# Performance work log

Hardware: AMD Instinct MI355X
Metric: run time of the kernel (lower is better)

Reference implementation:

```python
import jax, jax.numpy as jnp
import numpy as np

DIM = 128; MOTION = 128; HEADS = 8; WS = 8; B2 = 4; H = 192; W = 192; HID = 512

def _ln(x, w, b, eps=1e-5):
    m = x.mean(-1, keepdims=True)
    v = ((x - m) ** 2).mean(-1, keepdims=True)
    return (x - m) / jnp.sqrt(v + eps) * w + b

def _win_part(x, ws):
    B, Hh, Ww, C = x.shape
    x = x.reshape(B, Hh // ws, ws, Ww // ws, ws, C).transpose(0, 1, 3, 2, 4, 5)
    return x.reshape(-1, ws * ws, C)

def _win_rev(win, ws, Hh, Ww):
    nwB, N, C = win.shape
    B = nwB // ((Hh // ws) * (Ww // ws))
    x = win.reshape(B, Hh // ws, Ww // ws, ws, ws, C).transpose(0, 1, 3, 2, 4, 5)
    return x.reshape(B, Hh, Ww, C)

def setup_inputs() -> dict:
    key = jax.random.key(0)
    ks = jax.random.split(key, 12)
    def lin(k, o, i):
        return jax.random.normal(k, (o, i), jnp.float32) * 0.02
    return {
        "x": jax.random.normal(ks[0], (B2, H * W, DIM), jnp.float32),
        "cor": jax.random.uniform(ks[1], (B2, H * W, 2), dtype=jnp.float32),
        "q_w": lin(ks[2], DIM, DIM),
        "kv_w": lin(ks[3], 2 * DIM, DIM),
        "cor_w": lin(ks[4], MOTION, 2),
        "proj_w": lin(ks[5], DIM, DIM), "proj_b": jnp.zeros((DIM,), jnp.float32),
        "mproj_w": lin(ks[6], MOTION, MOTION), "mproj_b": jnp.zeros((MOTION,), jnp.float32),
        "norm1_w": jnp.ones((DIM,), jnp.float32), "norm1_b": jnp.zeros((DIM,), jnp.float32),
        "norm2_w": jnp.ones((DIM,), jnp.float32), "norm2_b": jnp.zeros((DIM,), jnp.float32),
        "fc1_w": lin(ks[7], HID, DIM), "fc1_b": jnp.zeros((HID,), jnp.float32),
        "dw_w": jax.random.normal(ks[8], (HID, 1, 3, 3), jnp.float32) * 0.1,
        "dw_b": jnp.zeros((HID,), jnp.float32),
        "fc2_w": lin(ks[9], DIM, HID), "fc2_b": jnp.zeros((DIM,), jnp.float32),
    }

def _attn(x1, x2, cor, q_w, kv_w, cor_w, proj_w, proj_b, mproj_w, mproj_b):
    # x1,x2: (nwB, N, C) windowed query / cross-frame key-value; cor: (nwB, N, 2)
    B, N, C = x1.shape
    hd = C // HEADS
    mh = MOTION // HEADS
    scale = hd ** -0.5
    q = (x1 @ q_w.T).reshape(B, N, HEADS, hd).transpose(0, 2, 1, 3)
    kv = (x2 @ kv_w.T).reshape(B, N, 2, HEADS, hd).transpose(2, 0, 3, 1, 4)
    k, v = kv[0], kv[1]
    ce = cor @ cor_w.T                                   # (B, N, MOTION)
    ceh = ce.reshape(B, N, HEADS, mh).transpose(0, 2, 1, 3)
    attn = jax.nn.softmax(jnp.einsum('bhnd,bhmd->bhnm', q, k) * scale, axis=-1)
    xo = jnp.einsum('bhnm,bhmd->bhnd', attn, v).transpose(0, 2, 1, 3).reshape(B, N, C)
    crev = jnp.einsum('bhnm,bhmd->bhnd', attn, ceh).transpose(0, 2, 1, 3).reshape(B, N, MOTION)
    motion = (crev - ce) @ mproj_w.T + mproj_b
    return xo @ proj_w.T + proj_b, motion

def _mlp(x, fc1_w, fc1_b, dw_w, dw_b, fc2_w, fc2_b):
    B, N, _ = x.shape
    h = x @ fc1_w.T + fc1_b                              # (B, N, HID)
    hm = h.transpose(0, 2, 1).reshape(B, HID, H, W)
    hm = jax.lax.conv_general_dilated(hm, dw_w, (1, 1), 'SAME',
                                      feature_group_count=HID,
                                      dimension_numbers=('NCHW', 'OIHW', 'NCHW'))
    hm = hm + dw_b[None, :, None, None]
    h = jax.nn.gelu(hm.reshape(B, HID, N).transpose(0, 2, 1), approximate=False)
    return h @ fc2_w.T + fc2_b

def reference(x, cor, q_w, kv_w, cor_w, proj_w, proj_b, mproj_w, mproj_b,
              norm1_w, norm1_b, norm2_w, norm2_b, fc1_w, fc1_b, dw_w, dw_b, fc2_w, fc2_b):
    shortcut = x
    xn = _ln(x, norm1_w, norm1_b).reshape(B2, H, W, DIM)
    cm = cor.reshape(B2, H, W, 2)
    xw = _win_part(xn, WS)                               # (nwB, 64, DIM)
    cw = _win_part(cm, WS)
    nwB = xw.shape[0]
    xr = jnp.concatenate([xw[nwB // 2:], xw[:nwB // 2]], axis=0)
    xa, xm = _attn(xw, xr, cw, q_w, kv_w, cor_w, proj_w, proj_b, mproj_w, mproj_b)
    xa = _win_rev(xa, WS, H, W).reshape(B2, H * W, DIM)
    xm = _win_rev(xm, WS, H, W).reshape(B2, H * W, MOTION)
    x = shortcut + xa
    x = x + _mlp(_ln(x, norm2_w, norm2_b), fc1_w, fc1_b, dw_w, dw_b, fc2_w, fc2_b)
    return x, xm
```

## Files before the change

### kernel.cpp

```cpp
#include <hip/hip_runtime.h>
#include <hip/hip_bf16.h>
#include <math.h>

#define NB 4
#define IMG 192
#define HW (IMG*IMG)
#define T_TOT (NB*HW)
#define HID 512
#define NWB 2304
#define WPB 576
#define NWS 24

typedef __bf16 bf16;
typedef __bf16 bf8 __attribute__((ext_vector_type(8)));
typedef __bf16 bf4 __attribute__((ext_vector_type(4)));
typedef float f32x4 __attribute__((ext_vector_type(4)));

#define MFMA(a,b,c) __builtin_amdgcn_mfma_f32_16x16x32_bf16(a,b,c,0,0,0)

__device__ __forceinline__ int swz128(int row, int col){ return row*128 + (col ^ ((row&7)<<3)); }

__device__ __forceinline__ bf8 zero_bf8(){
  bf8 z = { (bf16)0.f,(bf16)0.f,(bf16)0.f,(bf16)0.f,(bf16)0.f,(bf16)0.f,(bf16)0.f,(bf16)0.f };
  return z;
}
__device__ __forceinline__ f32x4 zero_f4(){ f32x4 z = {0.f,0.f,0.f,0.f}; return z; }

__global__ void k_cvt(const float* __restrict__ s, bf16* __restrict__ d, int n, float scale){
  int i = blockIdx.x*256 + threadIdx.x;
  if (i < n) d[i] = (bf16)(s[i]*scale);
}

__global__ void k_a2(const float* __restrict__ mproj_w, const float* __restrict__ cor_w,
                     bf16* __restrict__ a2w){
  int idx = blockIdx.x*256 + threadIdx.x;
  if (idx >= 4096) return;
  int o = idx >> 5, k = idx & 31;
  float acc = 0.f;
  if (k < 16){
    int h = k >> 1, c = k & 1;
    #pragma unroll
    for (int i=0;i<16;i++)
      acc += mproj_w[o*128 + h*16 + i] * cor_w[(h*16+i)*2 + c];
  }
  a2w[o*32 + k] = (bf16)acc;
}

__global__ __launch_bounds__(256) void k_ln1(
    const float* __restrict__ x, const float* __restrict__ cor,
    const float* __restrict__ n1w, const float* __restrict__ n1b,
    bf16* __restrict__ xn, bf16* __restrict__ cwb)
{
  int tid = threadIdx.x, wm = tid>>6, l = tid&63;
  int lr = l & 15, tg = l >> 4;
  int t = blockIdx.x*16 + wm*4 + tg;

  const float* xp = x + (size_t)t*128 + lr*8;
  float4 a = *(const float4*)xp;
  float4 b4 = *(const float4*)(xp+4);
  float s  = a.x+a.y+a.z+a.w + b4.x+b4.y+b4.z+b4.w;
  float sq = a.x*a.x+a.y*a.y+a.z*a.z+a.w*a.w + b4.x*b4.x+b4.y*b4.y+b4.z*b4.z+b4.w*b4.w;
  #pragma unroll
  for (int m=1;m<16;m<<=1){ s += __shfl_xor(s,m,16); sq += __shfl_xor(sq,m,16); }
  float mean = s * (1.0f/128.0f);
  float var  = sq * (1.0f/128.0f) - mean*mean;
  float rstd = rsqrtf(var + 1e-5f);

  float4 nw0 = *(const float4*)(n1w + lr*8), nw1 = *(const float4*)(n1w + lr*8 + 4);
  float4 nb0 = *(const float4*)(n1b + lr*8), nb1 = *(const float4*)(n1b + lr*8 + 4);

  bf8 o;
  o[0] = (bf16)((a.x -mean)*rstd*nw0.x + nb0.x);
  o[1] = (bf16)((a.y -mean)*rstd*nw0.y + nb0.y);
  o[2] = (bf16)((a.z -mean)*rstd*nw0.z + nb0.z);
  o[3] = (bf16)((a.w -mean)*rstd*nw0.w + nb0.w);
  o[4] = (bf16)((b4.x-mean)*rstd*nw1.x + nb1.x);
  o[5] = (bf16)((b4.y-mean)*rstd*nw1.y + nb1.y);
  o[6] = (bf16)((b4.z-mean)*rstd*nw1.z + nb1.z);
  o[7] = (bf16)((b4.w-mean)*rstd*nw1.w + nb1.w);

  int b = t / HW, r = t % HW;
  int yy = r / IMG, xx = r % IMG;
  int win = b*WPB + (yy>>3)*NWS + (xx>>3);
  int n = ((yy&7)<<3) + (xx&7);
  *(bf8*)(xn + (size_t)win*8192 + n*128 + lr*8) = o;

  if (lr < 2) cwb[(size_t)win*128 + n*2 + lr] = (bf16)cor[(size_t)t*2 + lr];
}

__global__ __launch_bounds__(256) void k_attn(
    const bf16* __restrict__ xn, const bf16* __restrict__ cw,
    const bf16* __restrict__ wq, const bf16* __restrict__ wkv,
    const bf16* __restrict__ wpj, const bf16* __restrict__ a2w,
    const float* __restrict__ proj_b, const float* __restrict__ mproj_b,
    const float* __restrict__ x_in, float* __restrict__ x1, float* __restrict__ out_m)
{
  __shared__ __align__(16) bf16 s_s [64*128];
  __shared__ __align__(16) bf16 s_k [64*128];
  __shared__ __align__(16) bf16 s_vT[128*64];
  __shared__ __align__(16) bf16 s_P [2][64*64];
  __shared__ __align__(16) bf16 s_cT[16*64];
  __shared__ __align__(16) bf16 s_D [64*32];

  int tid = threadIdx.x, wm = tid>>6, l = tid&63;
  int lr = l & 15, lg = l >> 4;
  int win = blockIdx.x;
  int partner = (win + NWB/2) % NWB;
  const bf16* xw_g = xn + (size_t)win*8192;
  const bf16* xr_g = xn + (size_t)partner*8192;

  bf8 xrv[4], xwv[4];
  #pragma unroll
  for (int tci=0;tci<4;tci++){
    int chunk = tid + tci*256;
    int row = chunk>>4, c0 = (chunk&15)*8;
    xrv[tci] = *(const bf8*)(xr_g + row*128 + c0);
    xwv[tci] = *(const bf8*)(xw_g + row*128 + c0);
  }
  bf16 cwv = (bf16)0.f;
  if (tid < 128) cwv = cw[(size_t)win*128 + tid];

  *(unsigned long long*)&s_cT[tid*4] = 0ull;
  *(unsigned long long*)&s_D[tid*8]   = 0ull;
  *(unsigned long long*)&s_D[tid*8+4] = 0ull;
  #pragma unroll
  for (int tci=0;tci<4;tci++){
    int chunk = tid + tci*256;
    int row = chunk>>4, c0 = (chunk&15)*8;
    *(bf8*)&s_s[swz128(row,c0)] = xrv[tci];
  }
  __syncthreads();

  if (tid < 128){
    int c = tid & 1, m = tid >> 1;
    s_cT[c*64 + (m ^ (c<<3))] = cwv;
  } else if (tid < 192){
    int m = tid - 128;
    s_cT[2*64 + (m ^ 16)] = (bf16)1.0f;
  }
  {
    bf8 af[4];
    #pragma unroll
    for (int ks=0;ks<4;ks++) af[ks] = *(const bf8*)&s_s[swz128(wm*16+lr, ks*32 + lg*8)];
    #pragma unroll
    for (int nt=0;nt<8;nt++){
      f32x4 acc = zero_f4();
      #pragma unroll
      for (int ks=0;ks<4;ks++){
        bf8 bfr = *(const bf8*)(wkv + (nt*16+lr)*128 + ks*32 + lg*8);
        acc = MFMA(af[ks], bfr, acc);
      }
      #pragma unroll
      for (int j=0;j<4;j++){
        int row = wm*16 + lg*4 + j;
        s_k[swz128(row, nt*16+lr)] = (bf16)acc[j];
      }
    }
    #pragma unroll
    for (int nt=0;nt<8;nt++){
      f32x4 acc = zero_f4();
      #pragma unroll
      for (int ks=0;ks<4;ks++){
        bf8 bfr = *(const bf8*)(wkv + (128 + nt*16+lr)*128 + ks*32 + lg*8);
        acc = MFMA(af[ks], bfr, acc);
      }
      #pragma unroll
      for (int j=0;j<4;j++){
        int tok = wm*16 + lg*4 + j;
        int chc = nt*16 + lr;
        s_vT[chc*64 + (tok ^ ((chc&7)<<3))] = (bf16)acc[j];
      }
    }
  }
  __syncthreads();

  #pragma unroll
  for (int tci=0;tci<4;tci++){
    int chunk = tid + tci*256;
    int row = chunk>>4, c0 = (chunk&15)*8;
    *(bf8*)&s_s[swz128(row,c0)] = xwv[tci];
  }
  __syncthreads();

  {
    bf8 af[4];
    #pragma unroll
    for (int ks=0;ks<4;ks++) af[ks] = *(const bf8*)&s_s[swz128(wm*16+lr, ks*32 + lg*8)];
    #pragma unroll
    for (int nt=0;nt<8;nt++){
      f32x4 acc = zero_f4();
      #pragma unroll
      for (int ks=0;ks<4;ks++){
        bf8 bfr = *(const bf8*)(wq + (nt*16+lr)*128 + ks*32 + lg*8);
        acc = MFMA(af[ks], bfr, acc);
      }
      #pragma unroll
      for (int j=0;j<4;j++){
        int row = wm*16 + lg*4 + j;
        s_s[swz128(row, nt*16+lr)] = (bf16)acc[j];
      }
    }
  }

  float mycw[4] = {0.f,0.f,0.f,0.f};
  if (lr < 2){
    #pragma unroll
    for (int j=0;j<4;j++){
      int row = wm*16 + lg*4 + j;
      mycw[j] = (float)s_cT[lr*64 + (row ^ (lr<<3))];
    }
  }

  #pragma unroll
  for (int h=0;h<8;h++){
    bf8 aS = zero_bf8();
    if (l < 32) aS = *(const bf8*)&s_s[swz128(wm*16+lr, h*16 + lg*8)];
    f32x4 accS[4];
    #pragma unroll
    for (int nt=0;nt<4;nt++){
      bf8 bSv = zero_bf8();
      if (l < 32) bSv = *(const bf8*)&s_k[swz128(nt*16+lr, h*16 + lg*8)];
      accS[nt] = MFMA(aS, bSv, zero_f4());
    }
    bf16* Pb = &s_P[h&1][0];
    #pragma unroll
    for (int nt=0;nt<4;nt++){
      #pragma unroll
      for (int j=0;j<4;j++){
        int row = wm*16 + lg*4 + j;
        Pb[row*64 + ((nt*16+lr) ^ ((row&7)<<3))] = (bf16)__expf(accS[nt][j]);
      }
    }
    f32x4 accO = zero_f4(), accPC = zero_f4();
    #pragma unroll
    for (int ks=0;ks<2;ks++){
      int rowA = wm*16 + lr;
      bf8 aP = *(const bf8*)&Pb[rowA*64 + ((ks*32 + lg*8) ^ ((rowA&7)<<3))];
      int chc = h*16 + lr;
      bf8 bV = *(const bf8*)&s_vT[chc*64 + ((ks*32 + lg*8) ^ ((chc&7)<<3))];
      accO = MFMA(aP, bV, accO);
      bf8 bC = *(const bf8*)&s_cT[lr*64 + ((ks*32 + lg*8) ^ ((lr&7)<<3))];
      accPC = MFMA(aP, bC, accPC);
    }
    #pragma unroll
    for (int j=0;j<4;j++){
      int row = wm*16 + lg*4 + j;
      float rs = __shfl(accPC[j], (l & 48) + 2, 64);
      float inv = __builtin_amdgcn_rcpf(rs);
      s_s[swz128(row, h*16+lr)] = (bf16)(accO[j]*inv);
      if (lr < 2)
        s_D[row*32 + ((2*h+lr) ^ ((row&3)<<3))] = (bf16)(accPC[j]*inv - mycw[j]);
    }
  }

  int b  = win / WPB, wi = win % WPB;
  int wy = wi / NWS,  wx = wi % NWS;
  {
    bf8 af[4];
    #pragma unroll
    for (int ks=0;ks<4;ks++) af[ks] = *(const bf8*)&s_s[swz128(wm*16+lr, ks*32 + lg*8)];
    #pragma unroll
    for (int nt=0;nt<8;nt++){
      f32x4 acc = zero_f4();
      #pragma unroll
      for (int ks=0;ks<4;ks++){
        bf8 bfr = *(const bf8*)(wpj + (nt*16+lr)*128 + ks*32 + lg*8);
        acc = MFMA(af[ks], bfr, acc);
      }
      int col = nt*16 + lr;
      float pb = proj_b[col];
      #pragma unroll
      for (int j=0;j<4;j++){
        int tok = wm*16 + lg*4 + j;
        int yy = wy*8 + (tok>>3), xx = wx*8 + (tok&7);
        size_t addr = ((size_t)b*HW + yy*IMG + xx)*128 + col;
        x1[addr] = acc[j] + pb + x_in[addr];
      }
    }
  }
  {
    int rowA = wm*16 + lr;
    bf8 afD = *(const bf8*)&s_D[rowA*32 + ((lg*8) ^ ((rowA&3)<<3))];
    #pragma unroll
    for (int nt=0;nt<8;nt++){
      bf8 bfr = *(const bf8*)(a2w + (nt*16+lr)*32 + lg*8);
      f32x4 acc = MFMA(afD, bfr, zero_f4());
      int col = nt*16 + lr;
      float pb = mproj_b[col];
      #pragma unroll
      for (int j=0;j<4;j++){
        int tok = wm*16 + lg*4 + j;
        int yy = wy*8 + (tok>>3), xx = wx*8 + (tok&7);
        size_t addr = ((size_t)b*HW + yy*IMG + xx)*128 + col;
        out_m[addr] = acc[j] + pb;
      }
    }
  }
}

__global__ __launch_bounds__(256) void k_fc1(
    const float* __restrict__ x1, const float* __restrict__ n2w, const float* __restrict__ n2b,
    const bf16* __restrict__ wf1, const float* __restrict__ fc1b, bf16* __restrict__ h)
{
  __shared__ __align__(16) bf16 s_a[64*128];
  int tid = threadIdx.x, wm = tid>>6, l = tid&63;
  int lr = l & 15, lg = l >> 4;
  size_t t0 = (size_t)blockIdx.x * 64;

  float4 nw0 = *(const float4*)(n2w + lr*8), nw1 = *(const float4*)(n2w + lr*8 + 4);
  float4 nb0 = *(const float4*)(n2b + lr*8), nb1 = *(const float4*)(n2b + lr*8 + 4);

  #pragma unroll
  for (int rr=0; rr<4; rr++){
    int row = wm*16 + rr*4 + lg;
    const float* xp = x1 + (t0+row)*128 + lr*8;
    float4 a = *(const float4*)xp;
    float4 b4 = *(const float4*)(xp+4);
    float s  = a.x+a.y+a.z+a.w + b4.x+b4.y+b4.z+b4.w;
    float sq = a.x*a.x+a.y*a.y+a.z*a.z+a.w*a.w + b4.x*b4.x+b4.y*b4.y+b4.z*b4.z+b4.w*b4.w;
    #pragma unroll
    for (int m=1;m<16;m<<=1){ s += __shfl_xor(s,m,16); sq += __shfl_xor(sq,m,16); }
    float mean = s*(1.f/128.f), var = sq*(1.f/128.f) - mean*mean;
    float rstd = rsqrtf(var + 1e-5f);
    bf8 o;
    o[0] = (bf16)((a.x -mean)*rstd*nw0.x + nb0.x);
    o[1] = (bf16)((a.y -mean)*rstd*nw0.y + nb0.y);
    o[2] = (bf16)((a.z -mean)*rstd*nw0.z + nb0.z);
    o[3] = (bf16)((a.w -mean)*rstd*nw0.w + nb0.w);
    o[4] = (bf16)((b4.x-mean)*rstd*nw1.x + nb1.x);
    o[5] = (bf16)((b4.y-mean)*rstd*nw1.y + nb1.y);
    o[6] = (bf16)((b4.z-mean)*rstd*nw1.z + nb1.z);
    o[7] = (bf16)((b4.w-mean)*rstd*nw1.w + nb1.w);
    *(bf8*)&s_a[swz128(row, lr*8)] = o;
  }
  __syncthreads();

  bf8 af[4];
  #pragma unroll
  for (int ks=0;ks<4;ks++) af[ks] = *(const bf8*)&s_a[swz128(wm*16+lr, ks*32 + lg*8)];
  for (int ntb=0; ntb<4; ntb++){
    f32x4 acc[8];
    #pragma unroll
    for (int q8=0;q8<8;q8++){
      acc[q8] = zero_f4();
      #pragma unroll
      for (int ks=0;ks<4;ks++){
        int ocol = ntb*128 + q8*16 + lr;
        bf8 bfr = *(const bf8*)(wf1 + (size_t)ocol*128 + ks*32 + lg*8);
        acc[q8] = MFMA(af[ks], bfr, acc[q8]);
      }
    }
    #pragma unroll
    for (int q8=0;q8<8;q8++){
      int col = ntb*128 + q8*16 + lr;
      float bb = fc1b[col];
      #pragma unroll
      for (int j=0;j<4;j++){
        int tl = wm*16 + lg*4 + j;
        h[(t0+tl)*512 + col] = (bf16)(acc[q8][j] + bb);
      }
    }
  }
}

__global__ __launch_bounds__(256) void k_mlp2(
    const bf16* __restrict__ h, const float* __restrict__ dww, const float* __restrict__ dwb,
    const bf16* __restrict__ wf2, const float* __restrict__ fc2b,
    const float* __restrict__ x1, float* __restrict__ outx)
{
  __shared__ __align__(16) bf16 s_hh[100*136];
  int tid = threadIdx.x, wm = tid>>6, l = tid&63;
  int lr = l & 15, lg = l >> 4;
  int tile = blockIdx.x, b = blockIdx.y;
  int ty = tile / 24, tx = tile % 24;
  int cq = (tid & 31) * 4;
  int tg = tid >> 5;

  f32x4 acc[8];
  #pragma unroll
  for (int q=0;q<8;q++) acc[q] = zero_f4();

  for (int kc=0;kc<4;kc++){
    __syncthreads();
    for (int it=0; it<7; it++){
      int idx = it*256 + tid;
      if (idx < 1600){
        int pos = idx>>4, c0 = (idx&15)*8;
        int hy = pos/10, hx = pos%10;
        int yy = ty*8 + hy - 1, xx = tx*8 + hx - 1;
        bf8 v;
        if (yy>=0 && yy<IMG && xx>=0 && xx<IMG)
          v = *(const bf8*)(h + ((size_t)b*HW + yy*IMG + xx)*512 + kc*128 + c0);
        else v = zero_bf8();
        *(bf8*)&s_hh[pos*136 + c0] = v;
      }
    }
    __syncthreads();
    int chg0 = kc*128 + cq;
    float4 bias4 = *(const float4*)(dwb + chg0);
    float cr[8][4];
    #pragma unroll
    for (int i=0;i<8;i++){ cr[i][0]=bias4.x; cr[i][1]=bias4.y; cr[i][2]=bias4.z; cr[i][3]=bias4.w; }
    #pragma unroll
    for (int dy=0;dy<3;dy++){
      #pragma unroll
      for (int dx=0;dx<3;dx++){
        int tq = dy*3+dx;
        float w0 = dww[(chg0+0)*9 + tq];
        float w1 = dww[(chg0+1)*9 + tq];
        float w2 = dww[(chg0+2)*9 + tq];
        float w3 = dww[(chg0+3)*9 + tq];
        #pragma unroll
        for (int i=0;i<8;i++){
          bf4 pv = *(const bf4*)&s_hh[((tg+dy)*10 + (i+dx))*136 + cq];
          cr[i][0] += (float)pv[0]*w0;
          cr[i][1] += (float)pv[1]*w1;
          cr[i][2] += (float)pv[2]*w2;
          cr[i][3] += (float)pv[3]*w3;
        }
      }
    }
    bf4 gout[8];
    #pragma unroll
    for (int i=0;i<8;i++){
      #pragma unroll
      for (int c=0;c<4;c++){
        float hv = cr[i][c];
        float hv2 = hv*hv;
        float v = hv * fmaf(hv2, -0.0713548353f, -1.5957691216f);
        float g = hv * __builtin_amdgcn_rcpf(1.0f + __expf(v));
        gout[i][c] = (bf16)g;
      }
    }
    __syncthreads();
    #pragma unroll
    for (int i=0;i<8;i++){
      int pos = (tg+1)*10 + (i+1);
      *(bf4*)&s_hh[pos*136 + (cq ^ (i<<3))] = gout[i];
    }
    {
      bf8 af[4];
      #pragma unroll
      for (int ks=0;ks<4;ks++){
        int tok = wm*16 + lr;
        int pos = ((tok>>3)+1)*10 + (tok&7) + 1;
        af[ks] = *(const bf8*)&s_hh[pos*136 + ((ks*32 + lg*8) ^ ((lr&7)<<3))];
      }
      #pragma unroll
      for (int q=0;q<8;q++){
        #pragma unroll
        for (int ks=0;ks<4;ks++){
          bf8 bfr = *(const bf8*)(wf2 + (size_t)(q*16+lr)*512 + kc*128 + ks*32 + lg*8);
          acc[q] = MFMA(af[ks], bfr, acc[q]);
        }
      }
    }
  }
  #pragma unroll
  for (int q=0;q<8;q++){
    int col = q*16 + lr;
    float bb = fc2b[col];
    #pragma unroll
    for (int j=0;j<4;j++){
      int tok = wm*16 + lg*4 + j;
      int yy = ty*8 + (tok>>3), xx = tx*8 + (tok&7);
      size_t addr = ((size_t)b*HW + yy*IMG + xx)*128 + col;
      outx[addr] = acc[q][j] + bb + x1[addr];
    }
  }
}

extern "C" void kernel_launch(void* const* d_in, const int* in_sizes, int n_in,
                              void* d_out, int out_size, void* d_ws, size_t ws_size,
                              hipStream_t stream)
{
  const float* x      = (const float*)d_in[0];
  const float* cor    = (const float*)d_in[1];
  const float* q_w    = (const float*)d_in[2];
  const float* kv_w   = (const float*)d_in[3];
  const float* cor_w  = (const float*)d_in[4];
  const float* proj_w = (const float*)d_in[5];
  const float* proj_b = (const float*)d_in[6];
  const float* mproj_w= (const float*)d_in[7];
  const float* mproj_b= (const float*)d_in[8];
  const float* n1w    = (const float*)d_in[9];
  const float* n1b    = (const float*)d_in[10];
  const float* n2w    = (const float*)d_in[11];
  const float* n2b    = (const float*)d_in[12];
  const float* fc1w   = (const float*)d_in[13];
  const float* fc1b   = (const float*)d_in[14];
  const float* dww    = (const float*)d_in[15];
  const float* dwb    = (const float*)d_in[16];
  const float* fc2w   = (const float*)d_in[17];
  const float* fc2b   = (const float*)d_in[18];
  float* out = (float*)d_out;

  char* ws = (char*)d_ws;
  bf16* wq   = (bf16*)(ws + 0);
  bf16* wkv  = (bf16*)(ws + 32768);
  bf16* wpj  = (bf16*)(ws + 98304);
  bf16* a2w  = (bf16*)(ws + 131072);
  bf16* wf1  = (bf16*)(ws + 139264);
  bf16* wf2  = (bf16*)(ws + 270336);
  bf16* xn   = (bf16*)(ws + 401408);
  bf16* cwb  = (bf16*)(ws + 38150144);
  float* x1  = (float*)(ws + 38739968);
  bf16* hbuf = (bf16*)(ws + 114237440);

  k_cvt<<<64,  256, 0, stream>>>(q_w,   wq,  16384, 0.25f);
  k_cvt<<<128, 256, 0, stream>>>(kv_w,  wkv, 32768, 1.0f);
  k_cvt<<<64,  256, 0, stream>>>(proj_w,wpj, 16384, 1.0f);
  k_cvt<<<256, 256, 0, stream>>>(fc1w,  wf1, 65536, 1.0f);
  k_cvt<<<256, 256, 0, stream>>>(fc2w,  wf2, 65536, 1.0f);
  k_a2 <<<16,  256, 0, stream>>>(mproj_w, cor_w, a2w);

  k_ln1 <<<T_TOT/16, 256, 0, stream>>>(x, cor, n1w, n1b, xn, cwb);
  k_attn<<<NWB,      256, 0, stream>>>(xn, cwb, wq, wkv, wpj, a2w, proj_b, mproj_b,
                                       x, x1, out + (size_t)T_TOT*128);
  k_fc1 <<<T_TOT/64, 256, 0, stream>>>(x1, n2w, n2b, wf1, fc1b, hbuf);
  k_mlp2<<<dim3(576,4), 256, 0, stream>>>(hbuf, dww, dwb, wf2, fc2b, x1, out);
}
```

Measured before the change: 568.2 us.

## Fuse LN2+fc1 into the depthwise-conv/fc2 MLP kernel with halo recompute

Merges the fc1 kernel into the conv/fc2 kernel. Each 8x8 tile now applies LayerNorm to a 10x10 halo of x1 and runs fc1 for all 100 positions, one 128-channel chunk at a time, into shared memory. This removes the global write and read of the 512-wide bf16 hidden buffer. In exchange, fc1 is recomputed on halo positions (about 1.56x the fc1 MFMA work), and shared memory per block roughly doubles, which may lower occupancy.

```diff
diff --git a/kernel.cpp b/kernel.cpp
--- a/kernel.cpp
+++ b/kernel.cpp
@@ -298,104 +298,109 @@
   }
 }
 
-__global__ __launch_bounds__(256) void k_fc1(
+__global__ __launch_bounds__(256) void k_mlp(
     const float* __restrict__ x1, const float* __restrict__ n2w, const float* __restrict__ n2b,
-    const bf16* __restrict__ wf1, const float* __restrict__ fc1b, bf16* __restrict__ h)
+    const bf16* __restrict__ wf1, const float* __restrict__ fc1b,
+    const float* __restrict__ dww, const float* __restrict__ dwb,
+    const bf16* __restrict__ wf2, const float* __restrict__ fc2b,
+    float* __restrict__ outx)
 {
-  __shared__ __align__(16) bf16 s_a[64*128];
-  int tid = threadIdx.x, wm = tid>>6, l = tid&63;
-  int lr = l & 15, lg = l >> 4;
-  size_t t0 = (size_t)blockIdx.x * 64;
-
-  float4 nw0 = *(const float4*)(n2w + lr*8), nw1 = *(const float4*)(n2w + lr*8 + 4);
-  float4 nb0 = *(const float4*)(n2b + lr*8), nb1 = *(const float4*)(n2b + lr*8 + 4);
-
-  #pragma unroll
-  for (int rr=0; rr<4; rr++){
-    int row = wm*16 + rr*4 + lg;
-    const float* xp = x1 + (t0+row)*128 + lr*8;
-    float4 a = *(const float4*)xp;
-    float4 b4 = *(const float4*)(xp+4);
-    float s  = a.x+a.y+a.z+a.w + b4.x+b4.y+b4.z+b4.w;
-    float sq = a.x*a.x+a.y*a.y+a.z*a.z+a.w*a.w + b4.x*b4.x+b4.y*b4.y+b4.z*b4.z+b4.w*b4.w;
-    #pragma unroll
-    for (int m=1;m<16;m<<=1){ s += __shfl_xor(s,m,16); sq += __shfl_xor(sq,m,16); }
-    float mean = s*(1.f/128.f), var = sq*(1.f/128.f) - mean*mean;
-    float rstd = rsqrtf(var + 1e-5f);
-    bf8 o;
-    o[0] = (bf16)((a.x -mean)*rstd*nw0.x + nb0.x);
-    o[1] = (bf16)((a.y -mean)*rstd*nw0.y + nb0.y);
-    o[2] = (bf16)((a.z -mean)*rstd*nw0.z + nb0.z);
-    o[3] = (bf16)((a.w -mean)*rstd*nw0.w + nb0.w);
-    o[4] = (bf16)((b4.x-mean)*rstd*nw1.x + nb1.x);
-    o[5] = (bf16)((b4.y-mean)*rstd*nw1.y + nb1.y);
-    o[6] = (bf16)((b4.z-mean)*rstd*nw1.z + nb1.z);
-    o[7] = (bf16)((b4.w-mean)*rstd*nw1.w + nb1.w);
-    *(bf8*)&s_a[swz128(row, lr*8)] = o;
-  }
-  __syncthreads();
-
-  bf8 af[4];
-  #pragma unroll
-  for (int ks=0;ks<4;ks++) af[ks] = *(const bf8*)&s_a[swz128(wm*16+lr, ks*32 + lg*8)];
-  for (int ntb=0; ntb<4; ntb++){
-    f32x4 acc[8];
-    #pragma unroll
-    for (int q8=0;q8<8;q8++){
-      acc[q8] = zero_f4();
-      #pragma unroll
-      for (int ks=0;ks<4;ks++){
-        int ocol = ntb*128 + q8*16 + lr;
-        bf8 bfr = *(const bf8*)(wf1 + (size_t)ocol*128 + ks*32 + lg*8);
-        acc[q8] = MFMA(af[ks], bfr, acc[q8]);
-      }
-    }
-    #pragma unroll
-    for (int q8=0;q8<8;q8++){
-      int col = ntb*128 + q8*16 + lr;
-      float bb = fc1b[col];
-      #pragma unroll
-      for (int j=0;j<4;j++){
-        int tl = wm*16 + lg*4 + j;
-        h[(t0+tl)*512 + col] = (bf16)(acc[q8][j] + bb);
-      }
-    }
-  }
-}
-
-__global__ __launch_bounds__(256) void k_mlp2(
-    const bf16* __restrict__ h, const float* __restrict__ dww, const float* __restrict__ dwb,
-    const bf16* __restrict__ wf2, const float* __restrict__ fc2b,
-    const float* __restrict__ x1, float* __restrict__ outx)
-{
-  __shared__ __align__(16) bf16 s_hh[100*136];
+  __shared__ __align__(16) bf16 s_x[112*128];
+  __shared__ __align__(16) bf16 s_h[112*128];
   int tid = threadIdx.x, wm = tid>>6, l = tid&63;
   int lr = l & 15, lg = l >> 4;
   int tile = blockIdx.x, b = blockIdx.y;
   int ty = tile / 24, tx = tile % 24;
+  bool edge = (ty==0) | (ty==23) | (tx==0) | (tx==23);
   int cq = (tid & 31) * 4;
-  int tg = tid >> 5;
-
-  f32x4 acc[8];
-  #pragma unroll
-  for (int q=0;q<8;q++) acc[q] = zero_f4();
+  int tg2 = tid >> 5;
+
+  {
+    float4 nw0 = *(const float4*)(n2w + lr*8), nw1 = *(const float4*)(n2w + lr*8 + 4);
+    float4 nb0 = *(const float4*)(n2b + lr*8), nb1 = *(const float4*)(n2b + lr*8 + 4);
+    int tq = tid >> 4;
+    #pragma unroll
+    for (int p=0;p<7;p++){
+      int tt = p*16 + tq;
+      if (tt < 100){
+        int hy = tt/10, hx = tt%10;
+        int yy = ty*8 + hy - 1, xx = tx*8 + hx - 1;
+        bool valid = (yy>=0) & (yy<IMG) & (xx>=0) & (xx<IMG);
+        int yya = valid ? yy : 0, xxa = valid ? xx : 0;
+        const float* xp = x1 + ((size_t)b*HW + yya*IMG + xxa)*128 + lr*8;
+        float4 a = *(const float4*)xp;
+        float4 b4 = *(const float4*)(xp+4);
+        float s  = a.x+a.y+a.z+a.w + b4.x+b4.y+b4.z+b4.w;
+        float sq = a.x*a.x+a.y*a.y+a.z*a.z+a.w*a.w + b4.x*b4.x+b4.y*b4.y+b4.z*b4.z+b4.w*b4.w;
+        #pragma unroll
+        for (int m=1;m<16;m<<=1){ s += __shfl_xor(s,m,16); sq += __shfl_xor(sq,m,16); }
+        float mean = s*(1.f/128.f), var = sq*(1.f/128.f) - mean*mean;
+        float rstd = rsqrtf(var + 1e-5f);
+        bf8 o;
+        o[0] = (bf16)((a.x -mean)*rstd*nw0.x + nb0.x);
+        o[1] = (bf16)((a.y -mean)*rstd*nw0.y + nb0.y);
+        o[2] = (bf16)((a.z -mean)*rstd*nw0.z + nb0.z);
+        o[3] = (bf16)((a.w -mean)*rstd*nw0.w + nb0.w);
+        o[4] = (bf16)((b4.x-mean)*rstd*nw1.x + nb1.x);
+        o[5] = (bf16)((b4.y-mean)*rstd*nw1.y + nb1.y);
+        o[6] = (bf16)((b4.z-mean)*rstd*nw1.z + nb1.z);
+        o[7] = (bf16)((b4.w-mean)*rstd*nw1.w + nb1.w);
+        *(bf8*)&s_x[swz128(tt, lr*8)] = o;
+      } else {
+        *(bf8*)&s_x[swz128(tt, lr*8)] = zero_bf8();
+      }
+    }
+  }
+  __syncthreads();
+
+  f32x4 acc2[8];
+  #pragma unroll
+  for (int q=0;q<8;q++) acc2[q] = zero_f4();
 
   for (int kc=0;kc<4;kc++){
+    if (kc) __syncthreads();
+
+    #pragma unroll
+    for (int mi=0; mi<2; mi++){
+      int mt = wm + mi*4;
+      if (mt < 7){
+        bf8 af[4];
+        #pragma unroll
+        for (int ks=0;ks<4;ks++) af[ks] = *(const bf8*)&s_x[swz128(mt*16+lr, ks*32 + lg*8)];
+        #pragma unroll
+        for (int nt=0;nt<8;nt++){
+          int ocol = kc*128 + nt*16 + lr;
+          f32x4 acc = zero_f4();
+          #pragma unroll
+          for (int ks=0;ks<4;ks++){
+            bf8 bfr = *(const bf8*)(wf1 + (size_t)ocol*128 + ks*32 + lg*8);
+            acc = MFMA(af[ks], bfr, acc);
+          }
+          float bb = fc1b[ocol];
+          #pragma unroll
+          for (int j=0;j<4;j++){
+            int row = mt*16 + lg*4 + j;
+            s_h[swz128(row, nt*16+lr)] = (bf16)(acc[j] + bb);
+          }
+        }
+      }
+    }
+    if (edge){
+      __syncthreads();
+      #pragma unroll
+      for (int it=0;it<7;it++){
+        int idx = it*256 + tid;
+        if (idx < 1600){
+          int pos = idx>>4, c0 = (idx&15)*8;
+          int hy = pos/10, hx = pos%10;
+          int yy = ty*8 + hy - 1, xx = tx*8 + hx - 1;
+          if (yy<0 || yy>=IMG || xx<0 || xx>=IMG)
+            *(bf8*)&s_h[swz128(pos, c0)] = zero_bf8();
+        }
+      }
+    }
     __syncthreads();
-    for (int it=0; it<7; it++){
-      int idx = it*256 + tid;
-      if (idx < 1600){
-        int pos = idx>>4, c0 = (idx&15)*8;
-        int hy = pos/10, hx = pos%10;
-        int yy = ty*8 + hy - 1, xx = tx*8 + hx - 1;
-        bf8 v;
-        if (yy>=0 && yy<IMG && xx>=0 && xx<IMG)
-          v = *(const bf8*)(h + ((size_t)b*HW + yy*IMG + xx)*512 + kc*128 + c0);
-        else v = zero_bf8();
-        *(bf8*)&s_hh[pos*136 + c0] = v;
-      }
-    }
-    __syncthreads();
+
     int chg0 = kc*128 + cq;
     float4 bias4 = *(const float4*)(dwb + chg0);
     float cr[8][4];
@@ -412,7 +417,7 @@
         float w3 = dww[(chg0+3)*9 + tq];
         #pragma unroll
         for (int i=0;i<8;i++){
-          bf4 pv = *(const bf4*)&s_hh[((tg+dy)*10 + (i+dx))*136 + cq];
+          bf4 pv = *(const bf4*)&s_h[swz128((tg2+dy)*10 + (i+dx), cq)];
           cr[i][0] += (float)pv[0]*w0;
           cr[i][1] += (float)pv[1]*w1;
           cr[i][2] += (float)pv[2]*w2;
@@ -434,24 +439,23 @@
     }
     __syncthreads();
     #pragma unroll
-    for (int i=0;i<8;i++){
-      int pos = (tg+1)*10 + (i+1);
-      *(bf4*)&s_hh[pos*136 + (cq ^ (i<<3))] = gout[i];
-    }
+    for (int i=0;i<8;i++)
+      *(bf4*)&s_h[swz128((tg2+1)*10 + (i+1), cq)] = gout[i];
+
     {
-      bf8 af[4];
+      bf8 af2[4];
       #pragma unroll
       for (int ks=0;ks<4;ks++){
         int tok = wm*16 + lr;
         int pos = ((tok>>3)+1)*10 + (tok&7) + 1;
-        af[ks] = *(const bf8*)&s_hh[pos*136 + ((ks*32 + lg*8) ^ ((lr&7)<<3))];
+        af2[ks] = *(const bf8*)&s_h[swz128(pos, ks*32 + lg*8)];
       }
       #pragma unroll
       for (int q=0;q<8;q++){
         #pragma unroll
         for (int ks=0;ks<4;ks++){
           bf8 bfr = *(const bf8*)(wf2 + (size_t)(q*16+lr)*512 + kc*128 + ks*32 + lg*8);
-          acc[q] = MFMA(af[ks], bfr, acc[q]);
+          acc2[q] = MFMA(af2[ks], bfr, acc2[q]);
         }
       }
     }
@@ -465,7 +469,7 @@
       int tok = wm*16 + lg*4 + j;
       int yy = ty*8 + (tok>>3), xx = tx*8 + (tok&7);
       size_t addr = ((size_t)b*HW + yy*IMG + xx)*128 + col;
-      outx[addr] = acc[q][j] + bb + x1[addr];
+      outx[addr] = acc2[q][j] + bb + x1[addr];
     }
   }
 }
@@ -505,7 +509,6 @@
   bf16* xn   = (bf16*)(ws + 401408);
   bf16* cwb  = (bf16*)(ws + 38150144);
   float* x1  = (float*)(ws + 38739968);
-  bf16* hbuf = (bf16*)(ws + 114237440);
 
   k_cvt<<<64,  256, 0, stream>>>(q_w,   wq,  16384, 0.25f);
   k_cvt<<<128, 256, 0, stream>>>(kv_w,  wkv, 32768, 1.0f);
@@ -517,6 +520,6 @@
   k_ln1 <<<T_TOT/16, 256, 0, stream>>>(x, cor, n1w, n1b, xn, cwb);
   k_attn<<<NWB,      256, 0, stream>>>(xn, cwb, wq, wkv, wpj, a2w, proj_b, mproj_b,
                                        x, x1, out + (size_t)T_TOT*128);
-  k_fc1 <<<T_TOT/64, 256, 0, stream>>>(x1, n2w, n2b, wf1, fc1b, hbuf);
-  k_mlp2<<<dim3(576,4), 256, 0, stream>>>(hbuf, dww, dwb, wf2, fc2b, x1, out);
-}
+  k_mlp <<<dim3(576,4), 256, 0, stream>>>(x1, n2w, n2b, wf1, fc1b, dww, dwb,
+                                          wf2, fc2b, out);
+}
```

After: 863.8 us. 52.0% more time.

## Prefetch next channel chunk into registers in fused dwconv+fc2 kernel

Applied to the files above, without the earlier changes.

The depthwise-conv/GELU/fc2 kernel now issues the global loads for the next 128-channel chunk of the hidden activations into registers before computing the current chunk, then writes them to shared memory after the MFMA stage. The goal is to hide global-memory latency behind the convolution and matrix work. It also reverses the block-to-tile mapping, probably for L2 locality with the preceding kernel. The price is 7 extra bf8 registers per thread, which may lower occupancy.

```diff
diff --git a/kernel.cpp b/kernel.cpp
--- a/kernel.cpp
+++ b/kernel.cpp
@@ -371,31 +371,46 @@
   __shared__ __align__(16) bf16 s_hh[100*136];
   int tid = threadIdx.x, wm = tid>>6, l = tid&63;
   int lr = l & 15, lg = l >> 4;
-  int tile = blockIdx.x, b = blockIdx.y;
+  int tile = 575 - blockIdx.x, b = 3 - blockIdx.y;
   int ty = tile / 24, tx = tile % 24;
   int cq = (tid & 31) * 4;
-  int tg = tid >> 5;
+  int tg2 = tid >> 5;
 
   f32x4 acc[8];
   #pragma unroll
   for (int q=0;q<8;q++) acc[q] = zero_f4();
 
+  bf8 stg[7];
+  #define STAGE_LOAD(KC)                                                     \
+    _Pragma("unroll")                                                        \
+    for (int it=0; it<7; it++){                                              \
+      int idx = it*256 + tid;                                                \
+      stg[it] = zero_bf8();                                                  \
+      if (idx < 1600){                                                       \
+        int pos = idx>>4, c0 = (idx&15)*8;                                   \
+        int hy = pos/10, hx = pos%10;                                        \
+        int yy = ty*8 + hy - 1, xx = tx*8 + hx - 1;                          \
+        if (yy>=0 && yy<IMG && xx>=0 && xx<IMG)                              \
+          stg[it] = *(const bf8*)(h + ((size_t)b*HW + yy*IMG + xx)*512 + (KC)*128 + c0); \
+      }                                                                      \
+    }
+  #define STAGE_WRITE()                                                      \
+    _Pragma("unroll")                                                        \
+    for (int it=0; it<7; it++){                                              \
+      int idx = it*256 + tid;                                                \
+      if (idx < 1600){                                                       \
+        int pos = idx>>4, c0 = (idx&15)*8;                                   \
+        *(bf8*)&s_hh[pos*136 + c0] = stg[it];                                \
+      }                                                                      \
+    }
+
+  STAGE_LOAD(0);
+  STAGE_WRITE();
+  __syncthreads();
+
   for (int kc=0;kc<4;kc++){
-    __syncthreads();
-    for (int it=0; it<7; it++){
-      int idx = it*256 + tid;
-      if (idx < 1600){
-        int pos = idx>>4, c0 = (idx&15)*8;
-        int hy = pos/10, hx = pos%10;
-        int yy = ty*8 + hy - 1, xx = tx*8 + hx - 1;
-        bf8 v;
-        if (yy>=0 && yy<IMG && xx>=0 && xx<IMG)
-          v = *(const bf8*)(h + ((size_t)b*HW + yy*IMG + xx)*512 + kc*128 + c0);
-        else v = zero_bf8();
-        *(bf8*)&s_hh[pos*136 + c0] = v;
-      }
-    }
-    __syncthreads();
+    if (kc < 3) STAGE_LOAD(kc+1);
+
     int chg0 = kc*128 + cq;
     float4 bias4 = *(const float4*)(dwb + chg0);
     float cr[8][4];
@@ -412,7 +427,7 @@
         float w3 = dww[(chg0+3)*9 + tq];
         #pragma unroll
         for (int i=0;i<8;i++){
-          bf4 pv = *(const bf4*)&s_hh[((tg+dy)*10 + (i+dx))*136 + cq];
+          bf4 pv = *(const bf4*)&s_hh[((tg2+dy)*10 + (i+dx))*136 + cq];
           cr[i][0] += (float)pv[0]*w0;
           cr[i][1] += (float)pv[1]*w1;
           cr[i][2] += (float)pv[2]*w2;
@@ -435,7 +450,7 @@
     __syncthreads();
     #pragma unroll
     for (int i=0;i<8;i++){
-      int pos = (tg+1)*10 + (i+1);
+      int pos = (tg2+1)*10 + (i+1);
       *(bf4*)&s_hh[pos*136 + (cq ^ (i<<3))] = gout[i];
     }
     {
@@ -455,6 +470,11 @@
         }
       }
     }
+    if (kc < 3){
+      __syncthreads();
+      STAGE_WRITE();
+      __syncthreads();
+    }
   }
   #pragma unroll
   for (int q=0;q<8;q++){
@@ -468,6 +488,8 @@
       outx[addr] = acc[q][j] + bb + x1[addr];
     }
   }
+  #undef STAGE_LOAD
+  #undef STAGE_WRITE
 }
 
 extern "C" void kernel_launch(void* const* d_in, const int* in_sizes, int n_in,
```

Measured after the change: 544.0 us. -4.3%, faster.

## Double-buffer MLP2 halo tiles with direct global-to-LDS async loads

Applied to the files above, without the earlier changes.

The depthwise-conv+fc2 kernel now keeps two LDS buffers and prefetches the next 128-channel chunk with global_load_lds DMA while computing the current one. Out-of-image halo positions are zero-filled once, and only for edge tiles. Each conv row is loaded from LDS into registers once and reused across the three dx taps. It also reverses block order, and the LDS row stride drops from 136 to 128, which may add bank conflicts. The aim is to hide global load latency; the cost is a doubled LDS footprint that could lower occupancy.

```diff
diff --git a/kernel.cpp b/kernel.cpp
--- a/kernel.cpp
+++ b/kernel.cpp
@@ -25,6 +25,12 @@
   return z;
 }
 __device__ __forceinline__ f32x4 zero_f4(){ f32x4 z = {0.f,0.f,0.f,0.f}; return z; }
+
+typedef const __attribute__((address_space(1))) unsigned int as1_u32;
+typedef __attribute__((address_space(3))) unsigned int as3_u32;
+__device__ __forceinline__ void gload16(const bf16* g, bf16* l){
+  __builtin_amdgcn_global_load_lds((as1_u32*)g, (as3_u32*)l, 16, 0, 0);
+}
 
 __global__ void k_cvt(const float* __restrict__ s, bf16* __restrict__ d, int n, float scale){
   int i = blockIdx.x*256 + threadIdx.x;
@@ -368,34 +374,56 @@
     const bf16* __restrict__ wf2, const float* __restrict__ fc2b,
     const float* __restrict__ x1, float* __restrict__ outx)
 {
-  __shared__ __align__(16) bf16 s_hh[100*136];
+  __shared__ __align__(16) bf16 s_hh[2][100*128];
   int tid = threadIdx.x, wm = tid>>6, l = tid&63;
   int lr = l & 15, lg = l >> 4;
-  int tile = blockIdx.x, b = blockIdx.y;
+  int tile = 575 - blockIdx.x, b = 3 - blockIdx.y;
   int ty = tile / 24, tx = tile % 24;
   int cq = (tid & 31) * 4;
-  int tg = tid >> 5;
+  int tg2 = tid >> 5;
 
   f32x4 acc[8];
   #pragma unroll
   for (int q=0;q<8;q++) acc[q] = zero_f4();
 
-  for (int kc=0;kc<4;kc++){
-    __syncthreads();
+  bool edge = (ty==0) | (ty==23) | (tx==0) | (tx==23);
+  if (edge){
+    #pragma unroll
     for (int it=0; it<7; it++){
       int idx = it*256 + tid;
       if (idx < 1600){
         int pos = idx>>4, c0 = (idx&15)*8;
         int hy = pos/10, hx = pos%10;
         int yy = ty*8 + hy - 1, xx = tx*8 + hx - 1;
-        bf8 v;
-        if (yy>=0 && yy<IMG && xx>=0 && xx<IMG)
-          v = *(const bf8*)(h + ((size_t)b*HW + yy*IMG + xx)*512 + kc*128 + c0);
-        else v = zero_bf8();
-        *(bf8*)&s_hh[pos*136 + c0] = v;
-      }
-    }
-    __syncthreads();
+        if (yy<0 || yy>=IMG || xx<0 || xx>=IMG){
+          *(bf8*)&s_hh[0][pos*128 + c0] = zero_bf8();
+          *(bf8*)&s_hh[1][pos*128 + c0] = zero_bf8();
+        }
+      }
+    }
+  }
+
+  #define STAGE_DMA(KC, BUF)                                                  \
+    _Pragma("unroll")                                                         \
+    for (int it=0; it<7; it++){                                               \
+      int idx = it*256 + tid;                                                 \
+      if (idx < 1600){                                                        \
+        int pos = idx>>4, c0 = (idx&15)*8;                                    \
+        int hy = pos/10, hx = pos%10;                                         \
+        int yy = ty*8 + hy - 1, xx = tx*8 + hx - 1;                           \
+        bf16* lb = &s_hh[BUF][it*2048 + wm*512];       \
+        if (yy>=0 && yy<IMG && xx>=0 && xx<IMG)                               \
+          gload16(h + ((size_t)b*HW + yy*IMG + xx)*512 + (KC)*128 + c0, lb);  \
+      }                                                                       \
+    }
+
+  STAGE_DMA(0, 0);
+  __syncthreads();
+
+  int cur = 0;
+  for (int kc=0;kc<4;kc++){
+    if (kc < 3) STAGE_DMA(kc+1, cur^1);
+
     int chg0 = kc*128 + cq;
     float4 bias4 = *(const float4*)(dwb + chg0);
     float cr[8][4];
@@ -403,6 +431,13 @@
     for (int i=0;i<8;i++){ cr[i][0]=bias4.x; cr[i][1]=bias4.y; cr[i][2]=bias4.z; cr[i][3]=bias4.w; }
     #pragma unroll
     for (int dy=0;dy<3;dy++){
+      float rv[10][4];
+      #pragma unroll
+      for (int p=0;p<10;p++){
+        bf4 pv = *(const bf4*)&s_hh[cur][((tg2+dy)*10 + p)*128 + cq];
+        rv[p][0]=(float)pv[0]; rv[p][1]=(float)pv[1];
+        rv[p][2]=(float)pv[2]; rv[p][3]=(float)pv[3];
+      }
       #pragma unroll
       for (int dx=0;dx<3;dx++){
         int tq = dy*3+dx;
@@ -412,11 +447,10 @@
         float w3 = dww[(chg0+3)*9 + tq];
         #pragma unroll
         for (int i=0;i<8;i++){
-          bf4 pv = *(const bf4*)&s_hh[((tg+dy)*10 + (i+dx))*136 + cq];
-          cr[i][0] += (float)pv[0]*w0;
-          cr[i][1] += (float)pv[1]*w1;
-          cr[i][2] += (float)pv[2]*w2;
-          cr[i][3] += (float)pv[3]*w3;
+          cr[i][0] += rv[i+dx][0]*w0;
+          cr[i][1] += rv[i+dx][1]*w1;
+          cr[i][2] += rv[i+dx][2]*w2;
+          cr[i][3] += rv[i+dx][3]*w3;
         }
       }
     }
@@ -435,8 +469,8 @@
     __syncthreads();
     #pragma unroll
     for (int i=0;i<8;i++){
-      int pos = (tg+1)*10 + (i+1);
-      *(bf4*)&s_hh[pos*136 + (cq ^ (i<<3))] = gout[i];
+      int pos = (tg2+1)*10 + (i+1);
+      *(bf4*)&s_hh[cur][pos*128 + (cq ^ (i<<3))] = gout[i];
     }
     {
       bf8 af[4];
@@ -444,7 +478,7 @@
       for (int ks=0;ks<4;ks++){
         int tok = wm*16 + lr;
         int pos = ((tok>>3)+1)*10 + (tok&7) + 1;
-        af[ks] = *(const bf8*)&s_hh[pos*136 + ((ks*32 + lg*8) ^ ((lr&7)<<3))];
+        af[ks] = *(const bf8*)&s_hh[cur][pos*128 + ((ks*32 + lg*8) ^ ((lr&7)<<3))];
       }
       #pragma unroll
       for (int q=0;q<8;q++){
@@ -455,6 +489,8 @@
         }
       }
     }
+    __syncthreads();
+    cur ^= 1;
   }
   #pragma unroll
   for (int q=0;q<8;q++){
@@ -468,6 +504,7 @@
       outx[addr] = acc[q][j] + bb + x1[addr];
     }
   }
+  #undef STAGE_DMA
 }
 
 extern "C" void kernel_launch(void* const* d_in, const int* in_sizes, int n_in,
```

New measurement: 541.3 us. 1.05x faster.
